# Kernel tuning notes

Hardware: AMD Instinct MI355X
Metric: run time of the kernel (lower is better)

Reference implementation:

```python
import jax, jax.numpy as jnp
import numpy as np
import math

KH = KW = 3
STRIDE = 1
PAD = 1
DIL = 1
C_IN = 256
C_OUT = 256
RANK = 32
BATCH = 16
H = W = 56


def setup_inputs() -> dict:
    key = jax.random.key(0)
    kx, kg, kh_, kb = jax.random.split(key, 4)
    x = jax.random.normal(kx, (BATCH, C_IN, H, W), dtype=jnp.float32)
    k2 = KH * KW
    bg = 1.0 / math.sqrt(C_IN)
    bh = 1.0 / math.sqrt(RANK)
    G = jax.random.uniform(kg, (k2, RANK, C_IN), minval=-bg, maxval=bg, dtype=jnp.float32)
    Hm = jax.random.uniform(kh_, (k2, C_OUT, RANK), minval=-bh, maxval=bh, dtype=jnp.float32)
    bias = jax.random.uniform(kb, (C_OUT,), minval=-bg, maxval=bg, dtype=jnp.float32)
    return {"x": x, "G": G, "Hm": Hm, "bias": bias}


def reference(x, G, Hm, bias):
    # Low-rank conv: per kernel position k, project patch through G[k] (rank) then H[k] (out),
    # then MEAN over the k2 positions (matches the original's .mean(dim=0)).
    b, c, h, w = x.shape
    h_out = (h + 2 * PAD - DIL * (KH - 1) - 1) // STRIDE + 1
    w_out = (h + 2 * PAD - DIL * (KW - 1) - 1) // STRIDE + 1  # original uses h here; square input
    xp = jnp.pad(x, ((0, 0), (0, 0), (PAD, PAD), (PAD, PAD)))
    acc = jnp.zeros((b, Hm.shape[1], h_out, w_out), dtype=x.dtype)
    for i in range(KH):
        for j in range(KW):
            k = i * KW + j
            # strided patch view for kernel offset (i, j): [b, c, h_out, w_out]
            patch = xp[:, :,
                       i * DIL:i * DIL + (h_out - 1) * STRIDE + 1:STRIDE,
                       j * DIL:j * DIL + (w_out - 1) * STRIDE + 1:STRIDE]
            t = jnp.einsum('bchw,rc->brhw', patch, G[k])      # rank projection
            acc = acc + jnp.einsum('brhw,or->bohw', t, Hm[k])  # out projection
    out = acc / (KH * KW) + bias[None, :, None, None]
    return out
```

## Files before the change

kernel.cpp:

```cpp
#include <hip/hip_runtime.h>
#include <stdint.h>


#define BATCH 16
#define CIN   256
#define COUT  256
#define RANK  32
#define HH    56
#define WW    56
#define SP    (HH*WW)
#define YP    58
#define XP    58
#define PCELL (YP*XP)
#define PLANE (BATCH*PCELL)

typedef __bf16 bf16x8 __attribute__((ext_vector_type(8)));
typedef __bf16 bf16x4 __attribute__((ext_vector_type(4)));
typedef float  f32x4  __attribute__((ext_vector_type(4)));

#define OFF_T9 0
#define OFF_GB 31002624
#define OFF_HB (OFF_GB + 147456)

#define RING_U4 (9 * 16 * 228 * 4)
#define PREP_N  (147456 + RING_U4)

__device__ __forceinline__ uint16_t bfbits(float f) {
  __bf16 h = (__bf16)f;
  return __builtin_bit_cast(uint16_t, h);
}

__global__ __launch_bounds__(256) void k_prep(const float* __restrict__ G,
                                              const float* __restrict__ Hm,
                                              uint16_t* __restrict__ G_bf,
                                              uint16_t* __restrict__ Hm_bf,
                                              uint16_t* __restrict__ T9) {
  int i = blockIdx.x * 256 + threadIdx.x;
  if (i < 73728)  { G_bf[i] = bfbits(G[i]); return; }
  if (i < 147456) { Hm_bf[i - 73728] = bfbits(Hm[i - 73728]); return; }
  int j = i - 147456;
  if (j >= RING_U4) return;
  int v = j & 3, cell = j >> 2;
  int tb = cell / 228, c = cell % 228;
  int y, xx;
  if      (c < 58)  { y = 0;       xx = c;       }
  else if (c < 116) { y = 57;      xx = c - 58;  }
  else if (c < 172) { y = c - 115; xx = 0;       }
  else              { y = c - 171; xx = 57;      }
  uint16_t* base = T9 + ((size_t)tb * PCELL + y * XP + xx) * 32;
  uint4 z; z.x = z.y = z.z = z.w = 0u;
  ((uint4*)base)[v] = z;
}

__global__ __launch_bounds__(384, 3) void k_fused1(const float* __restrict__ x,
                                                   const uint16_t* __restrict__ G_bf,
                                                   uint16_t* __restrict__ T9) {
  __shared__ uint16_t xs[32 * 264];
  const int tid = threadIdx.x;
  const int wave = tid >> 6, lane = tid & 63;
  const int q = lane >> 4, t = lane & 15;

  bf16x8 A[3][8];
  {
    const uint16_t* gb = G_bf + (size_t)(wave * 48 + t) * CIN + q * 8;
#pragma unroll
    for (int i = 0; i < 3; ++i)
#pragma unroll
      for (int ks = 0; ks < 8; ++ks)
        A[i][ks] = *(const bf16x8*)(gb + (size_t)i * 16 * CIN + ks * 32);
  }

#pragma unroll 1
  for (int item = blockIdx.x; item < 1568; item += 512) {
    const int b = item / 98, ch = item - b * 98;

#pragma unroll 1
    for (int u = tid; u < 512; u += 384) {
      const int s4 = u & 7, c4 = u >> 3;
      const int c0 = c4 * 4;
      const float* xr = x + ((size_t)(b * CIN + c0)) * SP + ch * 32 + s4 * 4;
      f32x4 f[4];
#pragma unroll
      for (int e = 0; e < 4; ++e)
        f[e] = *(const f32x4*)(xr + (size_t)e * SP);
#pragma unroll
      for (int p = 0; p < 4; ++p) {
        bf16x4 v;
#pragma unroll
        for (int e = 0; e < 4; ++e)
          ((__bf16*)&v)[e] = (__bf16)f[e][p];
        *(bf16x4*)&xs[(s4 * 4 + p) * 264 + c0] = v;
      }
    }
    __syncthreads();

#pragma unroll 1
    for (int nt = 0; nt < 2; ++nt) {
      bf16x8 Bf[8];
#pragma unroll
      for (int ks = 0; ks < 8; ++ks)
        Bf[ks] = *(const bf16x8*)&xs[(nt * 16 + t) * 264 + ks * 32 + q * 8];

      f32x4 acc[3];
#pragma unroll
      for (int i = 0; i < 3; ++i) acc[i] = (f32x4){0.f, 0.f, 0.f, 0.f};
#pragma unroll
      for (int ks = 0; ks < 8; ++ks)
#pragma unroll
        for (int i = 0; i < 3; ++i)
          acc[i] = __builtin_amdgcn_mfma_f32_16x16x32_bf16(A[i][ks], Bf[ks], acc[i], 0, 0, 0);

      const int p = ch * 32 + nt * 16 + t;
      const int h = p / WW, w = p - (p / WW) * WW;
      const size_t cellbase = ((size_t)b * PCELL + (h + 1) * XP + (w + 1)) * 32;
#pragma unroll
      for (int i = 0; i < 3; ++i) {
        const int kr0 = wave * 48 + i * 16 + q * 4;
        const int tap = kr0 >> 5, r = kr0 & 31;
        uint2 pv;
        pv.x = (uint32_t)bfbits(acc[i][0]) | ((uint32_t)bfbits(acc[i][1]) << 16);
        pv.y = (uint32_t)bfbits(acc[i][2]) | ((uint32_t)bfbits(acc[i][3]) << 16);
        *(uint2*)(T9 + (size_t)tap * PLANE * 32 + cellbase + r) = pv;
      }
    }
    __syncthreads();
  }
}

__global__ __launch_bounds__(512, 4) void k_stage2(const uint16_t* __restrict__ T9,
                                                   const uint16_t* __restrict__ Hm_bf,
                                                   const float* __restrict__ bias,
                                                   float* __restrict__ out) {
  const int wave = threadIdx.x >> 6, lane = threadIdx.x & 63;
  const int q = lane >> 4, t = lane & 15;

  bf16x8 Bf[9][2];
  float bv[2];
#pragma unroll
  for (int j = 0; j < 2; ++j) {
    const int o = wave * 32 + j * 16 + t;
    bv[j] = bias[o];
#pragma unroll
    for (int tap = 0; tap < 9; ++tap)
      Bf[tap][j] = *(const bf16x8*)(Hm_bf + ((size_t)(tap * COUT + o)) * RANK + q * 8);
  }

#pragma unroll 1
  for (int mt = blockIdx.x; mt < 3136; mt += 512) {
    const int p0 = mt * 16;
    const int b = p0 / SP, s0 = p0 - b * SP;
    const int sa = s0 + t;
    const int ha = sa / WW, wa = sa - ha * WW;
    const uint16_t* abase = T9 + ((size_t)(b * PCELL + ha * XP + wa)) * 32 + q * 8;

    f32x4 acc[2];
    acc[0] = (f32x4){0.f, 0.f, 0.f, 0.f};
    acc[1] = (f32x4){0.f, 0.f, 0.f, 0.f};
#pragma unroll
    for (int tap = 0; tap < 9; ++tap) {
      const int di = tap / 3, dj = tap % 3;
      bf16x8 af = *(const bf16x8*)(abase + (size_t)tap * PLANE * 32 + (di * XP + dj) * 32);
      acc[0] = __builtin_amdgcn_mfma_f32_16x16x32_bf16(af, Bf[0 + tap][0], acc[0], 0, 0, 0);
      acc[1] = __builtin_amdgcn_mfma_f32_16x16x32_bf16(af, Bf[0 + tap][1], acc[1], 0, 0, 0);
    }

    const int sd = s0 + q * 4;
#pragma unroll
    for (int j = 0; j < 2; ++j) {
      const int o = wave * 32 + j * 16 + t;
      f32x4 v = acc[j] * (1.0f / 9.0f) + bv[j];
      *(f32x4*)(out + ((size_t)(b * COUT + o)) * SP + sd) = v;
    }
  }
}

extern "C" void kernel_launch(void* const* d_in, const int* in_sizes, int n_in,
                              void* d_out, int out_size, void* d_ws, size_t ws_size,
                              hipStream_t stream) {
  const float* x    = (const float*)d_in[0];
  const float* G    = (const float*)d_in[1];
  const float* Hm   = (const float*)d_in[2];
  const float* bias = (const float*)d_in[3];
  float* out = (float*)d_out;
  char* ws = (char*)d_ws;

  uint16_t* T9    = (uint16_t*)(ws + OFF_T9);
  uint16_t* G_bf  = (uint16_t*)(ws + OFF_GB);
  uint16_t* Hm_bf = (uint16_t*)(ws + OFF_HB);

  k_prep<<<PREP_N / 256, 256, 0, stream>>>(G, Hm, G_bf, Hm_bf, T9);
  k_fused1<<<512, 384, 0, stream>>>(x, G_bf, T9);
  k_stage2<<<512, 512, 0, stream>>>(T9, Hm_bf, bias, out);
}
```

Before: 137.3 us.

## Double-buffer x tile in LDS and prefetch next item during MFMA compute

Stage 1 now issues the global loads for the next work item into registers before computing the current item, then writes them into a second LDS buffer after the MFMAs. This removes one barrier per item and hides global load latency behind compute. It also splits the B-fragment LDS loads into two halves to lower register pressure. The cost is double the LDS use and 32 extra live float registers, which may reduce occupancy under the 384x3 launch bound. Each block handles only about three items, so there is little to overlap.

```diff
diff --git a/kernel.cpp b/kernel.cpp
--- a/kernel.cpp
+++ b/kernel.cpp
@@ -55,11 +55,15 @@
 __global__ __launch_bounds__(384, 3) void k_fused1(const float* __restrict__ x,
                                                    const uint16_t* __restrict__ G_bf,
                                                    uint16_t* __restrict__ T9) {
-  __shared__ uint16_t xs[32 * 264];
+  __shared__ uint16_t xs[2][32 * 264];
   const int tid = threadIdx.x;
   const int wave = tid >> 6, lane = tid & 63;
   const int q = lane >> 4, t = lane & 15;
 
+  const int u0s4 = tid & 7,        u0c0 = (tid >> 3) * 4;
+  const int u1s4 = (tid + 384) & 7, u1c0 = ((tid + 384) >> 3) * 4;
+  const bool has_u1 = (tid < 128);
+
   bf16x8 A[3][8];
   {
     const uint16_t* gb = G_bf + (size_t)(wave * 48 + t) * CIN + q * 8;
@@ -70,45 +74,75 @@
         A[i][ks] = *(const bf16x8*)(gb + (size_t)i * 16 * CIN + ks * 32);
   }
 
-#pragma unroll 1
-  for (int item = blockIdx.x; item < 1568; item += 512) {
+  f32x4 f0[4], f1[4];
+
+  int item = blockIdx.x;
+  {
     const int b = item / 98, ch = item - b * 98;
-
-#pragma unroll 1
-    for (int u = tid; u < 512; u += 384) {
-      const int s4 = u & 7, c4 = u >> 3;
-      const int c0 = c4 * 4;
-      const float* xr = x + ((size_t)(b * CIN + c0)) * SP + ch * 32 + s4 * 4;
-      f32x4 f[4];
-#pragma unroll
-      for (int e = 0; e < 4; ++e)
-        f[e] = *(const f32x4*)(xr + (size_t)e * SP);
+    const float* xr0 = x + ((size_t)(b * CIN + u0c0)) * SP + ch * 32 + u0s4 * 4;
+#pragma unroll
+    for (int e = 0; e < 4; ++e) f0[e] = *(const f32x4*)(xr0 + (size_t)e * SP);
+    if (has_u1) {
+      const float* xr1 = x + ((size_t)(b * CIN + u1c0)) * SP + ch * 32 + u1s4 * 4;
+#pragma unroll
+      for (int e = 0; e < 4; ++e) f1[e] = *(const f32x4*)(xr1 + (size_t)e * SP);
+    }
+#pragma unroll
+    for (int p = 0; p < 4; ++p) {
+      bf16x4 v;
+#pragma unroll
+      for (int e = 0; e < 4; ++e) ((__bf16*)&v)[e] = (__bf16)f0[e][p];
+      *(bf16x4*)&xs[0][(u0s4 * 4 + p) * 264 + u0c0] = v;
+    }
+    if (has_u1) {
 #pragma unroll
       for (int p = 0; p < 4; ++p) {
         bf16x4 v;
 #pragma unroll
-        for (int e = 0; e < 4; ++e)
-          ((__bf16*)&v)[e] = (__bf16)f[e][p];
-        *(bf16x4*)&xs[(s4 * 4 + p) * 264 + c0] = v;
-      }
-    }
-    __syncthreads();
-
+        for (int e = 0; e < 4; ++e) ((__bf16*)&v)[e] = (__bf16)f1[e][p];
+        *(bf16x4*)&xs[0][(u1s4 * 4 + p) * 264 + u1c0] = v;
+      }
+    }
+  }
+  __syncthreads();
+
+  int cur = 0;
+#pragma unroll 1
+  for (; item < 1568; item += 512) {
+    const int nxt = item + 512;
+
+    if (nxt < 1568) {
+      const int bn = nxt / 98, chn = nxt - bn * 98;
+      const float* xr0 = x + ((size_t)(bn * CIN + u0c0)) * SP + chn * 32 + u0s4 * 4;
+#pragma unroll
+      for (int e = 0; e < 4; ++e) f0[e] = *(const f32x4*)(xr0 + (size_t)e * SP);
+      if (has_u1) {
+        const float* xr1 = x + ((size_t)(bn * CIN + u1c0)) * SP + chn * 32 + u1s4 * 4;
+#pragma unroll
+        for (int e = 0; e < 4; ++e) f1[e] = *(const f32x4*)(xr1 + (size_t)e * SP);
+      }
+    }
+
+    const int b = item / 98, ch = item - b * 98;
+    const uint16_t* xb = xs[cur];
 #pragma unroll 1
     for (int nt = 0; nt < 2; ++nt) {
-      bf16x8 Bf[8];
-#pragma unroll
-      for (int ks = 0; ks < 8; ++ks)
-        Bf[ks] = *(const bf16x8*)&xs[(nt * 16 + t) * 264 + ks * 32 + q * 8];
-
       f32x4 acc[3];
 #pragma unroll
       for (int i = 0; i < 3; ++i) acc[i] = (f32x4){0.f, 0.f, 0.f, 0.f};
 #pragma unroll
-      for (int ks = 0; ks < 8; ++ks)
-#pragma unroll
-        for (int i = 0; i < 3; ++i)
-          acc[i] = __builtin_amdgcn_mfma_f32_16x16x32_bf16(A[i][ks], Bf[ks], acc[i], 0, 0, 0);
+      for (int kh = 0; kh < 2; ++kh) {
+        bf16x8 Bf[4];
+#pragma unroll
+        for (int k4 = 0; k4 < 4; ++k4)
+          Bf[k4] = *(const bf16x8*)&xb[(nt * 16 + t) * 264 + (kh * 4 + k4) * 32 + q * 8];
+#pragma unroll
+        for (int k4 = 0; k4 < 4; ++k4)
+#pragma unroll
+          for (int i = 0; i < 3; ++i)
+            acc[i] = __builtin_amdgcn_mfma_f32_16x16x32_bf16(A[i][kh * 4 + k4], Bf[k4],
+                                                             acc[i], 0, 0, 0);
+      }
 
       const int p = ch * 32 + nt * 16 + t;
       const int h = p / WW, w = p - (p / WW) * WW;
@@ -123,7 +157,28 @@
         *(uint2*)(T9 + (size_t)tap * PLANE * 32 + cellbase + r) = pv;
       }
     }
+
+    if (nxt < 1568) {
+      uint16_t* xw = xs[cur ^ 1];
+#pragma unroll
+      for (int p = 0; p < 4; ++p) {
+        bf16x4 v;
+#pragma unroll
+        for (int e = 0; e < 4; ++e) ((__bf16*)&v)[e] = (__bf16)f0[e][p];
+        *(bf16x4*)&xw[(u0s4 * 4 + p) * 264 + u0c0] = v;
+      }
+      if (has_u1) {
+#pragma unroll
+        for (int p = 0; p < 4; ++p) {
+          bf16x4 v;
+#pragma unroll
+          for (int e = 0; e < 4; ++e) ((__bf16*)&v)[e] = (__bf16)f1[e][p];
+          *(bf16x4*)&xw[(u1s4 * 4 + p) * 264 + u1c0] = v;
+        }
+      }
+    }
     __syncthreads();
+    cur ^= 1;
   }
 }
 
```

After: 143.3 us. 1.04x slower.
